# Kernel optimization log

Measured on AMD Instinct MI355X. Metric: run time of the kernel, lower is better.

## Reference

```python
import jax, jax.numpy as jnp
import numpy as np

B_SZ, C, H, W = 64, 256, 28, 28
HEADS, HEAD_DIM = 4, 64
BLOCK, HALO = 4, 4
WIN = BLOCK + 2 * HALO  # 12
KCONV = 3


def _unfold(x, k, s, p):
    # torch F.unfold semantics; returns [b, c, oh, kh, ow, kw]
    b, c, h, w = x.shape
    xp = jnp.pad(x, ((0, 0), (0, 0), (p, p), (p, p)))
    oh = (h + 2 * p - k) // s + 1
    ow = (w + 2 * p - k) // s + 1
    ih = jnp.arange(oh)[:, None] * s + jnp.arange(k)[None, :]
    iw = jnp.arange(ow)[:, None] * s + jnp.arange(k)[None, :]
    pt = xp[:, :, ih]            # [b,c,oh,kh,Wp]
    pt = pt[:, :, :, :, iw]      # [b,c,oh,kh,ow,kw]
    return pt


def _rel_to_abs(x):
    # x: [b, l, 2r-1] -> [b, l, r] via shift trick
    b, l, m = x.shape
    r = (m + 1) // 2
    x = jnp.pad(x, ((0, 0), (0, 0), (0, 1))).reshape(b, l * (m + 1))
    x = jnp.pad(x, ((0, 0), (0, m - l))).reshape(b, l + 1, m)
    return x[:, :l, -r:]


def _relative_logits_1d(q, rel_k):
    # q: [b, x, y, d], rel_k: [2r-1, d] -> [b, x, i(=r), y, j(=r)]
    b, h, w, _ = q.shape
    r = (rel_k.shape[0] + 1) // 2
    logits = jnp.einsum('bxyd,rd->bxyr', q, rel_k)
    logits = _rel_to_abs(logits.reshape(b * h, w, 2 * r - 1)).reshape(b, h, w, r)
    return jnp.broadcast_to(logits[:, :, None], (b, h, r, w, r))


def _rel_pos_emb(q, rel_height, rel_width):
    # q: [B, block^2, d]
    B, n, d = q.shape
    qb = q.reshape(B, BLOCK, BLOCK, d)
    lw = _relative_logits_1d(qb, rel_width)                 # [B,x,i,y,j]
    lw = lw.transpose(0, 1, 3, 2, 4).reshape(B, n, -1)      # b (x y) (i j)
    qh = qb.transpose(0, 2, 1, 3)
    lh = _relative_logits_1d(qh, rel_height)                # [B,y,i,x,j]
    lh = lh.transpose(0, 3, 1, 4, 2).reshape(B, n, -1)      # b (y x) (j i)
    return lw + lh


def setup_inputs() -> dict:
    key = jax.random.key(0)
    ks = jax.random.split(key, 13)
    f = jnp.float32
    rel_scale = HEAD_DIM ** (-0.5)
    return {
        'x': jax.random.normal(ks[0], (B_SZ, C, H, W), dtype=f),
        'w1': jax.random.normal(ks[1], (C, C), dtype=f) * 0.05,
        'b1': jax.random.normal(ks[2], (C,), dtype=f) * 0.05,
        'w2': jax.random.normal(ks[3], (C, C), dtype=f) * 0.05,
        'b2': jax.random.normal(ks[4], (C,), dtype=f) * 0.05,
        'w3': jax.random.normal(ks[5], (C, C), dtype=f) * 0.05,
        'b3': jax.random.normal(ks[6], (C,), dtype=f) * 0.05,
        'fc_w': jax.random.normal(ks[7], (KCONV * KCONV, 3 * HEADS), dtype=f) * 0.1,
        'dep_w': jax.random.normal(ks[8], (C, KCONV * KCONV, KCONV, KCONV), dtype=f) * 0.05,
        'rel_height': jax.random.normal(ks[9], (2 * WIN - 1, HEAD_DIM), dtype=f) * rel_scale,
        'rel_width': jax.random.normal(ks[10], (2 * WIN - 1, HEAD_DIM), dtype=f) * rel_scale,
        'rate1': jax.random.normal(ks[11], (1,), dtype=f),
        'rate2': jax.random.normal(ks[12], (1,), dtype=f),
    }


def reference(x, w1, b1, w2, b2, w3, b3, fc_w, dep_w, rel_height, rel_width, rate1, rate2):
    b = x.shape[0]
    scaling = HEAD_DIM ** (-0.5)
    q = jnp.einsum('bchw,oc->bohw', x, w1) + b1[None, :, None, None]
    k = jnp.einsum('bchw,oc->bohw', x, w2) + b2[None, :, None, None]
    v = jnp.einsum('bchw,oc->bohw', x, w3) + b3[None, :, None, None]
    c = q.shape[1]
    nb = H // BLOCK          # 7 blocks per side
    nwin = nb * nb           # 49 windows
    n_q = BLOCK * BLOCK      # 16 queries per window
    n_k = WIN * WIN          # 144 keys per window (with halo)

    # block queries: b c (h p1) (w p2) -> (b h w) (p1 p2) c
    q_att = q.reshape(b, c, nb, BLOCK, nb, BLOCK).transpose(0, 2, 4, 3, 5, 1).reshape(b * nwin, n_q, c)
    kp = _unfold(k, WIN, BLOCK, HALO).transpose(0, 2, 4, 3, 5, 1).reshape(b * nwin, n_k, c)
    vp = _unfold(v, WIN, BLOCK, HALO).transpose(0, 2, 4, 3, 5, 1).reshape(b * nwin, n_k, c)

    def split_heads(t):
        Bn, n, _ = t.shape
        return t.reshape(Bn, n, HEADS, HEAD_DIM).transpose(0, 2, 1, 3).reshape(Bn * HEADS, n, HEAD_DIM)

    q1 = split_heads(q_att) * scaling
    k1 = split_heads(kp)
    v1 = split_heads(vp)

    sim = jnp.einsum('bid,bjd->bij', q1, k1)
    sim = sim + _rel_pos_emb(q1, rel_height, rel_width)

    # NOTE: faithfully reproduces original (valid positions get -max, padded get 0)
    ones = jnp.ones((1, 1, H, W), x.dtype)
    valid = _unfold(ones, WIN, BLOCK, HALO).transpose(0, 2, 4, 3, 5, 1).reshape(nwin, n_k) > 0
    big_neg = -jnp.finfo(sim.dtype).max
    sim = sim.reshape(b, nwin, HEADS, n_q, n_k)
    sim = jnp.where(valid[None, :, None, None, :], big_neg, sim)
    attn = jax.nn.softmax(sim, axis=-1).reshape(b * nwin * HEADS, n_q, n_k)

    out = jnp.einsum('bij,bjd->bid', attn, v1)
    out = out.reshape(b * nwin, HEADS, n_q, HEAD_DIM).transpose(0, 2, 1, 3)  # merge heads
    out = out.reshape(b, nb, nb, BLOCK, BLOCK, c)
    out_att = out.transpose(0, 5, 1, 3, 2, 4).reshape(b, c, H, W)

    # conv branch: fc over concatenated per-head q,k,v, then depthwise-grouped conv
    f_all = jnp.concatenate([
        q.reshape(b, HEADS, HEAD_DIM, H * W),
        k.reshape(b, HEADS, HEAD_DIM, H * W),
        v.reshape(b, HEADS, HEAD_DIM, H * W)], axis=1)        # [b, 3*heads, hd, HW]
    f_all = jnp.einsum('bcmn,oc->bomn', f_all, fc_w)          # [b, 9, hd, HW]
    f_conv = f_all.transpose(0, 2, 1, 3).reshape(b, HEAD_DIM * KCONV * KCONV, H, W)
    out_conv = jax.lax.conv_general_dilated(
        f_conv, dep_w, window_strides=(1, 1), padding=((1, 1), (1, 1)),
        dimension_numbers=('NCHW', 'OIHW', 'NCHW'), feature_group_count=HEAD_DIM)

    return rate1[0] * out_att + rate2[0] * out_conv
```

## Files before the change

### kernel.cpp

```cpp
#include <hip/hip_runtime.h>
#include <hip/hip_bf16.h>

typedef __hip_bfloat16 bf16;
typedef unsigned int uint;
typedef unsigned short ushort;

using frag8 = __attribute__((ext_vector_type(8))) short;
using f32x4 = __attribute__((ext_vector_type(4))) float;

#define HWH 784
#define PPITCH 30
#define PPLANE 900
#define PBLK 10800

__global__ __launch_bounds__(256) void prep(const float* __restrict__ x,
                                            const float* __restrict__ w1,
                                            const float* __restrict__ w2,
                                            const float* __restrict__ w3,
                                            const float* __restrict__ b1,
                                            const float* __restrict__ b2,
                                            const float* __restrict__ b3,
                                            const float* __restrict__ fc_w,
                                            const float* __restrict__ dep_w,
                                            bf16* __restrict__ xT,
                                            bf16* __restrict__ wbf,
                                            float* __restrict__ W2,
                                            float* __restrict__ biascat) {
    __shared__ float t[32][33];
    const int bid = blockIdx.x, tid = threadIdx.x;

    if (bid < 12800) {
        const int n0 = (bid % 25) * 32;
        const int c0 = ((bid / 25) % 8) * 32;
        const int b  = bid / 200;
        const float* xb = x + (size_t)b * (256 * HWH);
#pragma unroll
        for (int e = tid; e < 1024; e += 256) {
            int r = e >> 5, col = e & 31;
            int n = n0 + col;
            t[r][col] = (n < HWH) ? xb[(size_t)(c0 + r) * HWH + n] : 0.f;
        }
        __syncthreads();
#pragma unroll
        for (int e = tid; e < 512; e += 256) {
            int r = e >> 4, cp = (e & 15) * 2;
            int n = n0 + r;
            if (n < HWH) {
                __hip_bfloat162 h;
                h.x = __float2bfloat16(t[cp][r]);
                h.y = __float2bfloat16(t[cp + 1][r]);
                *reinterpret_cast<__hip_bfloat162*>(
                    &xT[((size_t)b * HWH + n) * 256 + c0 + cp]) = h;
            }
        }
        return;
    }

    if (bid < 13568) {
        const int row = bid - 12800;
        const float* src = row < 256 ? w1 : (row < 512 ? w2 : w3);
        wbf[row * 256 + tid] = __float2bfloat16(src[(row & 255) * 256 + tid]);
        return;
    }

    int idx = (bid - 13568) * 256 + tid;
    if (idx < 768) {
        const float* bs = idx < 256 ? b1 : (idx < 512 ? b2 : b3);
        biascat[idx] = bs[idx & 255];
    }
    if (idx >= 256 * 108) return;
    int oc  = idx / 108;
    int r   = idx % 108;
    int c12 = r / 9;
    int k9  = r % 9;
    float s = 0.f;
#pragma unroll
    for (int o = 0; o < 9; ++o)
        s += fc_w[o * 12 + c12] * dep_w[oc * 81 + o * 9 + k9];
    W2[idx] = s;
}

__device__ inline void load_lds16(const bf16* g, short* lds) {
    __builtin_amdgcn_global_load_lds(
        (const __attribute__((address_space(1))) void*)g,
        (__attribute__((address_space(3))) void*)lds, 16, 0, 0);
}

__global__ __launch_bounds__(256) void gemm_mfma(const bf16* __restrict__ wbf,
                                                 const float* __restrict__ biascat,
                                                 const bf16* __restrict__ xT,
                                                 bf16* __restrict__ perm) {
    __shared__ short lds[8192];

    const int tid  = threadIdx.x;
    const int wave = tid >> 6, lane = tid & 63;

    const int s  = blockIdx.x;
    const int X  = s & 7, jj = s >> 3;
    const int G  = X * 56 + jj / 6;
    const int mt = jj % 6;
    const int nt = G % 7;
    const int b  = G / 7;

    const int m0   = mt * 128;
    const int n0   = nt * 128;
    const int mw   = wave & 1, nw = wave >> 1;
    const int lrow = lane & 15, lkc = lane >> 4;

    f32x4 acc[4][4] = {};
    const bf16* xb = xT + (size_t)b * (HWH * 256);

    for (int k0 = 0; k0 < 256; k0 += 32) {
#pragma unroll
        for (int i = 0; i < 2; ++i) {
            const int jb = 2 * wave + i;
            const bf16* ga = wbf + (size_t)(m0 + 16 * jb + lrow) * 256 + k0 + lkc * 8;
            load_lds16(ga, &lds[jb * 512]);
            int n = n0 + 16 * jb + lrow;
            if (n > HWH - 1) n = HWH - 1;
            const bf16* gb = xb + (size_t)n * 256 + k0 + lkc * 8;
            load_lds16(gb, &lds[4096 + jb * 512]);
        }
        __syncthreads();

        frag8 af[4], bf_[4];
#pragma unroll
        for (int i = 0; i < 4; ++i)
            af[i] = *reinterpret_cast<const frag8*>(&lds[(4 * mw + i) * 512 + lane * 8]);
#pragma unroll
        for (int j2 = 0; j2 < 4; ++j2)
            bf_[j2] = *reinterpret_cast<const frag8*>(&lds[4096 + (4 * nw + j2) * 512 + lane * 8]);
#pragma unroll
        for (int i = 0; i < 4; ++i)
#pragma unroll
            for (int j2 = 0; j2 < 4; ++j2)
                acc[i][j2] = __builtin_amdgcn_mfma_f32_16x16x32_bf16(
                    af[i], bf_[j2], acc[i][j2], 0, 0, 0);
        __syncthreads();
    }

#pragma unroll
    for (int i = 0; i < 4; ++i) {
        const int rowb = m0 + mw * 64 + i * 16 + lkc * 4;
        bf16* base[4]; float bias4[4];
#pragma unroll
        for (int r = 0; r < 4; ++r) {
            const int m = rowb + r;
            const int sec = m >> 8, ch = m & 255;
            base[r] = perm + ((size_t)b * 64 + (ch & 63)) * PBLK
                           + (size_t)(sec * 4 + (ch >> 6)) * PPLANE;
            bias4[r] = biascat[m];
        }
#pragma unroll
        for (int j2 = 0; j2 < 4; ++j2) {
            const int col = n0 + nw * 64 + j2 * 16 + lrow;
            if (col < HWH) {
                const int pos = col + 2 * (col / 28) + 31;
#pragma unroll
                for (int r = 0; r < 4; ++r)
                    base[r][pos] = __float2bfloat16(acc[i][j2][r] + bias4[r]);
            }
        }
    }
}

__global__ __launch_bounds__(256) void attmean(const bf16* __restrict__ perm,
                                               const float* __restrict__ rate1,
                                               float* __restrict__ attm) {
    const int b = blockIdx.y, cg = blockIdx.x;
    const int wave = threadIdx.x >> 6, lane = threadIdx.x & 63;
    const int c = cg * 4 + wave;
    const bf16* vp = perm + ((size_t)(b * 64 + (c & 63)) * 12 + 8 + (c >> 6)) * (size_t)PPLANE;

    float cs[5] = {0.f, 0.f, 0.f, 0.f, 0.f};
    if (lane < 28) {
#pragma unroll
        for (int y = 0; y < 28; ++y) {
            float v = __bfloat162float(vp[(y + 1) * PPITCH + lane + 1]);
#pragma unroll
            for (int wi = 0; wi < 5; ++wi)
                if (y >= 4 * wi && y <= 4 * wi + 11) cs[wi] += v;
        }
    }
    const float r1s = rate1[0] * (1.0f / 144.0f);
#pragma unroll
    for (int wi = 0; wi < 5; ++wi) {
        float p = cs[wi];
#pragma unroll
        for (int d = 1; d < 32; d <<= 1) {
            float t = __shfl_up(p, d);
            if (lane >= d) p += t;
        }
        float hi = __shfl(p, 4 * lane + 11);
        float lo = __shfl(p, 4 * lane - 1);
        if (lane < 5) {
            float w = hi - (lane ? lo : 0.f);
            attm[((size_t)b * 256 + c) * 25 + wi * 5 + lane] = w * r1s;
        }
    }
}

__global__ __launch_bounds__(256) void out_fused5(
    const bf16* __restrict__ perm, const float* __restrict__ W2,
    const float* __restrict__ attm, const float* __restrict__ rate2,
    float* __restrict__ out) {
    __shared__ __align__(16) short planes[12 * PPLANE];
    __shared__ float w2s[4][12][12];
    __shared__ float attbs[4][25];

    const int g = blockIdx.x, b = blockIdx.y, tid = threadIdx.x;

    const uint4* src = (const uint4*)(perm + (size_t)(b * 64 + g) * PBLK);
#pragma unroll
    for (int it = 0; it < 6; ++it) {
        int e = tid + it * 256;
        if (e < 1350) ((uint4*)planes)[e] = src[e];
    }
    for (int e = tid; e < 576; e += 256) {
        int oc = e / 144, rem = e % 144, cc = rem / 12, k = rem % 12;
        w2s[oc][cc][k] = (k < 9) ? W2[(4 * g + oc) * 108 + cc * 9 + k] : 0.f;
    }
    if (tid < 100)
        attbs[tid / 25][tid % 25] =
            attm[((size_t)b * 256 + 4 * g + tid / 25) * 25 + tid % 25];
    __syncthreads();

    for (int e = tid; e < 1392; e += 256) {
        int c12 = e / 116, u = e % 116, idx;
        if (u < 30)      idx = u;
        else if (u < 60) idx = 870 + (u - 30);
        else { int v = u - 60; idx = ((v >> 1) + 1) * PPITCH + (v & 1) * 29; }
        planes[c12 * PPLANE + idx] = 0;
    }
    __syncthreads();

    float acc[4][4] = {};
    const int y = tid % 28, xs = tid / 28, x0 = xs * 4;
    if (tid < 196) {
#pragma unroll 1
        for (int c = 0; c < 12; ++c) {
            float rr[3][6];
#pragma unroll
            for (int dy = 0; dy < 3; ++dy) {
                const uint* row = (const uint*)&planes[c * PPLANE + (y + dy) * PPITCH + x0];
#pragma unroll
                for (int jp = 0; jp < 3; ++jp) {
                    uint w = row[jp];
                    float2 f = __bfloat1622float2(*(const __hip_bfloat162*)&w);
                    rr[dy][2 * jp]     = f.x;
                    rr[dy][2 * jp + 1] = f.y;
                }
            }
#pragma unroll
            for (int oc = 0; oc < 4; ++oc) {
                const float4* wr = reinterpret_cast<const float4*>(&w2s[oc][c][0]);
                float4 wa = wr[0], wb = wr[1], wc = wr[2];
                const float wk[9] = {wa.x, wa.y, wa.z, wa.w, wb.x, wb.y, wb.z, wb.w, wc.x};
#pragma unroll
                for (int ky = 0; ky < 3; ++ky)
#pragma unroll
                    for (int kx = 0; kx < 3; ++kx) {
                        float wv = wk[ky * 3 + kx];
#pragma unroll
                        for (int px = 0; px < 4; ++px)
                            acc[oc][px] += wv * rr[ky][px + kx];
                    }
            }
        }

        const float r2 = rate2[0];
        const int wi = (y >> 2) - 1, wj = xs - 1;
        const bool inter = (wi >= 0) & (wi < 5) & (wj >= 0) & (wj < 5);
#pragma unroll
        for (int oc = 0; oc < 4; ++oc) {
            float av = inter ? attbs[oc][wi * 5 + wj] : 0.f;
            float4 o;
            o.x = av + r2 * acc[oc][0];
            o.y = av + r2 * acc[oc][1];
            o.z = av + r2 * acc[oc][2];
            o.w = av + r2 * acc[oc][3];
            *reinterpret_cast<float4*>(
                &out[((size_t)(b * 256 + 4 * g + oc)) * HWH + y * 28 + x0]) = o;
        }
    }
}

extern "C" void kernel_launch(void* const* d_in, const int* in_sizes, int n_in,
                              void* d_out, int out_size, void* d_ws, size_t ws_size,
                              hipStream_t stream) {
    const float* x     = (const float*)d_in[0];
    const float* w1    = (const float*)d_in[1];
    const float* b1    = (const float*)d_in[2];
    const float* w2    = (const float*)d_in[3];
    const float* b2    = (const float*)d_in[4];
    const float* w3    = (const float*)d_in[5];
    const float* b3    = (const float*)d_in[6];
    const float* fc_w  = (const float*)d_in[7];
    const float* dep_w = (const float*)d_in[8];
    const float* rate1 = (const float*)d_in[11];
    const float* rate2 = (const float*)d_in[12];
    float* out = (float*)d_out;

    char* wsb = (char*)d_ws;
    bf16*  perm    = (bf16*)wsb;
    bf16*  xT      = (bf16*)(wsb + 88473600);
    float* attm    = (float*)(wsb + 88473600);
    bf16*  wbf     = (bf16*)(wsb + 114163712);
    float* W2      = (float*)(wsb + 114556928);
    float* biascat = (float*)(wsb + 114667520);

    prep      <<<dim3(13676),      dim3(256), 0, stream>>>(x, w1, w2, w3, b1, b2, b3,
                                                           fc_w, dep_w, xT, wbf, W2, biascat);
    gemm_mfma <<<dim3(2688),       dim3(256), 0, stream>>>(wbf, biascat, xT, perm);
    attmean   <<<dim3(64, 64),     dim3(256), 0, stream>>>(perm, rate1, attm);
    out_fused5<<<dim3(64, 64),     dim3(256), 0, stream>>>(perm, W2, attm, rate2, out);
}
```

Before: 249.4 us.

## Compute window means of x in prep and project through w3 in output kernel

The attmean kernel summed the bf16 V projection per window. It is replaced by window-sum means of raw x, computed in extra prep blocks. The output kernel now applies w3 and b3 to those means, using linearity of the value projection. This drops one kernel launch and its read of the V planes, but adds a 256-length dot product per output channel and window in each output block. It also reads full-precision x instead of bf16 V, which changes rounding slightly.

```diff
diff --git a/kernel.cpp b/kernel.cpp
--- a/kernel.cpp
+++ b/kernel.cpp
@@ -25,7 +25,8 @@
                                             bf16* __restrict__ xT,
                                             bf16* __restrict__ wbf,
                                             float* __restrict__ W2,
-                                            float* __restrict__ biascat) {
+                                            float* __restrict__ biascat,
+                                            float* __restrict__ sbar) {
     __shared__ float t[32][33];
     const int bid = blockIdx.x, tid = threadIdx.x;
 
@@ -63,21 +64,59 @@
         return;
     }
 
-    int idx = (bid - 13568) * 256 + tid;
-    if (idx < 768) {
-        const float* bs = idx < 256 ? b1 : (idx < 512 ? b2 : b3);
-        biascat[idx] = bs[idx & 255];
-    }
-    if (idx >= 256 * 108) return;
-    int oc  = idx / 108;
-    int r   = idx % 108;
-    int c12 = r / 9;
-    int k9  = r % 9;
-    float s = 0.f;
-#pragma unroll
-    for (int o = 0; o < 9; ++o)
-        s += fc_w[o * 12 + c12] * dep_w[oc * 81 + o * 9 + k9];
-    W2[idx] = s;
+    if (bid < 13676) {
+        int idx = (bid - 13568) * 256 + tid;
+        if (idx < 768) {
+            const float* bs = idx < 256 ? b1 : (idx < 512 ? b2 : b3);
+            biascat[idx] = bs[idx & 255];
+        }
+        if (idx >= 256 * 108) return;
+        int oc  = idx / 108;
+        int r   = idx % 108;
+        int c12 = r / 9;
+        int k9  = r % 9;
+        float s = 0.f;
+#pragma unroll
+        for (int o = 0; o < 9; ++o)
+            s += fc_w[o * 12 + c12] * dep_w[oc * 81 + o * 9 + k9];
+        W2[idx] = s;
+        return;
+    }
+
+    {
+        const int q  = bid - 13676;
+        const int b  = q >> 6, cg = q & 63;
+        const int wave = tid >> 6, lane = tid & 63;
+        const int c  = cg * 4 + wave;
+        const float* xp = x + ((size_t)b * 256 + c) * HWH;
+
+        float cs[5] = {0.f, 0.f, 0.f, 0.f, 0.f};
+        if (lane < 28) {
+#pragma unroll
+            for (int y = 0; y < 28; ++y) {
+                float v = xp[y * 28 + lane];
+#pragma unroll
+                for (int wi = 0; wi < 5; ++wi)
+                    if (y >= 4 * wi && y <= 4 * wi + 11) cs[wi] += v;
+            }
+        }
+#pragma unroll
+        for (int wi = 0; wi < 5; ++wi) {
+            float p = cs[wi];
+#pragma unroll
+            for (int d = 1; d < 32; d <<= 1) {
+                float t2 = __shfl_up(p, d);
+                if (lane >= d) p += t2;
+            }
+            float hi = __shfl(p, 4 * lane + 11);
+            float lo = __shfl(p, 4 * lane - 1);
+            if (lane < 5) {
+                float w = hi - (lane ? lo : 0.f);
+                sbar[((size_t)b * 25 + wi * 5 + lane) * 256 + c] =
+                    w * (1.0f / 144.0f);
+            }
+        }
+    }
 }
 
 __device__ inline void load_lds16(const bf16* g, short* lds) {
@@ -164,46 +203,11 @@
     }
 }
 
-__global__ __launch_bounds__(256) void attmean(const bf16* __restrict__ perm,
-                                               const float* __restrict__ rate1,
-                                               float* __restrict__ attm) {
-    const int b = blockIdx.y, cg = blockIdx.x;
-    const int wave = threadIdx.x >> 6, lane = threadIdx.x & 63;
-    const int c = cg * 4 + wave;
-    const bf16* vp = perm + ((size_t)(b * 64 + (c & 63)) * 12 + 8 + (c >> 6)) * (size_t)PPLANE;
-
-    float cs[5] = {0.f, 0.f, 0.f, 0.f, 0.f};
-    if (lane < 28) {
-#pragma unroll
-        for (int y = 0; y < 28; ++y) {
-            float v = __bfloat162float(vp[(y + 1) * PPITCH + lane + 1]);
-#pragma unroll
-            for (int wi = 0; wi < 5; ++wi)
-                if (y >= 4 * wi && y <= 4 * wi + 11) cs[wi] += v;
-        }
-    }
-    const float r1s = rate1[0] * (1.0f / 144.0f);
-#pragma unroll
-    for (int wi = 0; wi < 5; ++wi) {
-        float p = cs[wi];
-#pragma unroll
-        for (int d = 1; d < 32; d <<= 1) {
-            float t = __shfl_up(p, d);
-            if (lane >= d) p += t;
-        }
-        float hi = __shfl(p, 4 * lane + 11);
-        float lo = __shfl(p, 4 * lane - 1);
-        if (lane < 5) {
-            float w = hi - (lane ? lo : 0.f);
-            attm[((size_t)b * 256 + c) * 25 + wi * 5 + lane] = w * r1s;
-        }
-    }
-}
-
-__global__ __launch_bounds__(256) void out_fused5(
+__global__ __launch_bounds__(256) void out_fused6(
     const bf16* __restrict__ perm, const float* __restrict__ W2,
-    const float* __restrict__ attm, const float* __restrict__ rate2,
-    float* __restrict__ out) {
+    const float* __restrict__ sbar, const float* __restrict__ w3,
+    const float* __restrict__ b3, const float* __restrict__ rate1,
+    const float* __restrict__ rate2, float* __restrict__ out) {
     __shared__ __align__(16) short planes[12 * PPLANE];
     __shared__ float w2s[4][12][12];
     __shared__ float attbs[4][25];
@@ -220,9 +224,18 @@
         int oc = e / 144, rem = e % 144, cc = rem / 12, k = rem % 12;
         w2s[oc][cc][k] = (k < 9) ? W2[(4 * g + oc) * 108 + cc * 9 + k] : 0.f;
     }
-    if (tid < 100)
-        attbs[tid / 25][tid % 25] =
-            attm[((size_t)b * 256 + 4 * g + tid / 25) * 25 + tid % 25];
+    if (tid < 100) {
+        const int w = tid >> 2, oc = tid & 3;
+        const float4* sv = (const float4*)(sbar + ((size_t)b * 25 + w) * 256);
+        const float4* wv = (const float4*)(w3 + (size_t)(4 * g + oc) * 256);
+        float s = 0.f;
+#pragma unroll 8
+        for (int i = 0; i < 64; ++i) {
+            float4 a = sv[i], q = wv[i];
+            s += a.x * q.x + a.y * q.y + a.z * q.z + a.w * q.w;
+        }
+        attbs[oc][w] = rate1[0] * (s + b3[4 * g + oc]);
+    }
     __syncthreads();
 
     for (int e = tid; e < 1392; e += 256) {
@@ -304,14 +317,15 @@
     char* wsb = (char*)d_ws;
     bf16*  perm    = (bf16*)wsb;
     bf16*  xT      = (bf16*)(wsb + 88473600);
-    float* attm    = (float*)(wsb + 88473600);
     bf16*  wbf     = (bf16*)(wsb + 114163712);
     float* W2      = (float*)(wsb + 114556928);
     float* biascat = (float*)(wsb + 114667520);
-
-    prep      <<<dim3(13676),      dim3(256), 0, stream>>>(x, w1, w2, w3, b1, b2, b3,
-                                                           fc_w, dep_w, xT, wbf, W2, biascat);
+    float* sbar    = (float*)(wsb + 114670592);
+
+    prep      <<<dim3(17772),      dim3(256), 0, stream>>>(x, w1, w2, w3, b1, b2, b3,
+                                                           fc_w, dep_w, xT, wbf, W2,
+                                                           biascat, sbar);
     gemm_mfma <<<dim3(2688),       dim3(256), 0, stream>>>(wbf, biascat, xT, perm);
-    attmean   <<<dim3(64, 64),     dim3(256), 0, stream>>>(perm, rate1, attm);
-    out_fused5<<<dim3(64, 64),     dim3(256), 0, stream>>>(perm, W2, attm, rate2, out);
-}
+    out_fused6<<<dim3(64, 64),     dim3(256), 0, stream>>>(perm, W2, sbar, w3, b3,
+                                                           rate1, rate2, out);
+}
```

Result: slower. 283.8 us (+13.8%).
